# Optimization experiments

Measured on AMD Instinct MI355X. Metric: run time of the kernel, lower is better.

Reference implementation:

```python
import jax, jax.numpy as jnp
import numpy as np

B, L, C, R, DK = 8, 2048, 512, 64, 64
H = 2 * C  # hdnSize
NEG = -32767.0  # -2**15 + 1
EPS = 1e-5


def _p(key, shape, std=0.02):
    return (jax.random.normal(key, shape, dtype=jnp.float32) * std)


def setup_inputs() -> dict:
    key = jax.random.key(0)
    ks = jax.random.split(key, 16)
    inp = {
        "x": jax.random.normal(ks[0], (B, L, C), dtype=jnp.float32),
        "maskPAD": jax.random.randint(ks[1], (B, 1, L), 0, 2, dtype=jnp.int32),
        "preScores": jax.random.normal(ks[2], (B, R, R), dtype=jnp.float32),
        "Wp": _p(ks[3], (C, R)), "bp": jnp.zeros((R,), jnp.float32),
        "Wq": _p(ks[4], (C, DK)), "bq": jnp.zeros((DK,), jnp.float32),
        "Wk": _p(ks[5], (C, DK)), "bk": jnp.zeros((DK,), jnp.float32),
        "Wv": _p(ks[6], (C, H)), "bv": jnp.zeros((H,), jnp.float32),
        "Wu": _p(ks[7], (C, H)), "bu": jnp.zeros((H,), jnp.float32),
        "Wo": _p(ks[8], (H, C)), "bo": jnp.zeros((C,), jnp.float32),
        "gamma": jnp.ones((C,), jnp.float32),
        "beta": jnp.zeros((C,), jnp.float32),
    }
    return inp


def reference(x, maskPAD, preScores, Wp, bp, Wq, bq, Wk, bk, Wv, bv, Wu, bu, Wo, bo, gamma, beta):
    # GLU gate: [B,L,H]
    gate = jax.nn.silu(x @ Wu + bu)
    # pseudo-attention logits [B,L,r], masked on padded positions
    pScore = x @ Wp + bp
    pad = (maskPAD[:, 0] == 0)[..., None]  # [B,L,1]
    pScore = jnp.where(pad, NEG, pScore)
    pAlpha = jax.nn.softmax(pScore, axis=1)    # softmax over L (dim=-2)
    pAlpha_ = jax.nn.softmax(pScore, axis=-1)  # softmax over r
    # compress: px [B,r,C]  (== pAlpha.transpose(-1,-2) @ x)
    px = jnp.einsum('blr,blc->brc', pAlpha, x)
    q = jax.nn.silu(px @ Wq + bq)  # [B,r,dk]
    k = jax.nn.silu(px @ Wk + bk)  # [B,r,dk]
    v = jax.nn.silu(px @ Wv + bv)  # [B,r,H]
    scores = jnp.einsum('brd,bsd->brs', q, k) / np.sqrt(DK).astype(np.float32)
    scores = scores + preScores
    alpha = jax.nn.softmax(scores, axis=2)
    z = alpha @ v                                # [B,r,H]
    z = jnp.einsum('blr,brh->blh', pAlpha_, z)   # expand back to [B,L,H]
    z = gate * z
    z = z @ Wo + bo                              # [B,L,C]
    y = x + z
    mu = jnp.mean(y, axis=-1, keepdims=True)
    var = jnp.var(y, axis=-1, keepdims=True)
    out = (y - mu) * jax.lax.rsqrt(var + EPS) * gamma + beta
    return out
```

## Files before the change

kernel.cpp:

```cpp
#include <hip/hip_runtime.h>
#include <hip/hip_bf16.h>

constexpr int B_ = 8;
constexpr int L_ = 2048;
constexpr int C_ = 512;
constexpr int R_ = 64;
constexpr int DK_ = 64;
constexpr int H_ = 1024;
constexpr int M_ = B_ * L_;
constexpr int NQKV_ = 1152;
constexpr float NEG_ = -32767.0f;

__device__ __forceinline__ float toF(float x) { return x; }
__device__ __forceinline__ float toF(__hip_bfloat16 x) { return __bfloat162float(x); }
__device__ __forceinline__ float siluf(float v) { return v / (1.0f + __expf(-v)); }
__device__ __forceinline__ ushort bfbits(float f) {
    __hip_bfloat16 h = __float2bfloat16(f);
    union { __hip_bfloat16 h; ushort u; } cv; cv.h = h; return cv.u;
}
__device__ __forceinline__ float bf2f(ushort u) {
    union { uint u; float f; } cv; cv.u = (uint)u << 16; return cv.f;
}

typedef __attribute__((ext_vector_type(8))) short bf16x8;
typedef __attribute__((ext_vector_type(4))) float f32x4;

#define GLOBAL_AS __attribute__((address_space(1)))
#define LDS_AS    __attribute__((address_space(3)))
__device__ __forceinline__ void glds16(const ushort* g, ushort* l) {
    __builtin_amdgcn_global_load_lds((const GLOBAL_AS void*)g, (LDS_AS void*)l, 16, 0, 0);
}

#define VMCNT(n) asm volatile("s_waitcnt vmcnt(" #n ")" ::: "memory")
#define BARRIER() do { __builtin_amdgcn_s_barrier(); asm volatile("" ::: "memory"); } while (0)

template <int EPI>
__global__ __launch_bounds__(256) void mfma_gemm5(
    const ushort* __restrict__ A, const ushort* __restrict__ Bt,
    const float* __restrict__ bias,
    const float* __restrict__ residF, const ushort* __restrict__ residB,
    const int* __restrict__ mask,
    ushort* __restrict__ outB, float* __restrict__ outF, float* __restrict__ outF2,
    int Ndim, int Kdim, int gridN, long bBatch)
{
    __shared__ ushort As[3][128 * 32];
    __shared__ ushort Bs[3][128 * 32];

    const int i = blockIdx.x;
    const int G = gridDim.x >> 3;
    const int gi = (gridDim.x & 7) ? i : ((i & 7) * G + (i >> 3));
    const int nt = gi % gridN, mt = gi / gridN;
    const int m0 = mt * 128, n0 = nt * 128;

    const int tid = threadIdx.x;
    const int lane = tid & 63, w = tid >> 6;
    const int wm = (w & 1) * 64, wn = (w >> 1) * 64;
    const int lr = lane & 15, lq = lane >> 4;

    const int sr = lane >> 2;
    const int sc = (lane & 3) * 8;
    const int s0 = w * 2, s1 = w * 2 + 1;

    const ushort* Bp = Bt + (bBatch ? (long)(m0 / L_) * bBatch : 0);
    int br0 = n0 + s0 * 16 + sr; if (br0 >= Ndim) br0 = Ndim - 1;
    int br1 = n0 + s1 * 16 + sr; if (br1 >= Ndim) br1 = Ndim - 1;
    const ushort* a0p = A  + (size_t)(m0 + s0 * 16 + sr) * Kdim + sc;
    const ushort* a1p = A  + (size_t)(m0 + s1 * 16 + sr) * Kdim + sc;
    const ushort* b0p = Bp + (size_t)br0 * Kdim + sc;
    const ushort* b1p = Bp + (size_t)br1 * Kdim + sc;
    const int lo0 = s0 * 512 + lane * 8;
    const int lo1 = s1 * 512 + lane * 8;

    f32x4 acc[4][4];
#pragma unroll
    for (int a = 0; a < 4; ++a)
#pragma unroll
        for (int b = 0; b < 4; ++b) acc[a][b] = (f32x4){0.f, 0.f, 0.f, 0.f};

    glds16(a0p, &As[0][lo0]);
    glds16(a1p, &As[0][lo1]);
    glds16(b0p, &Bs[0][lo0]);
    glds16(b1p, &Bs[0][lo1]);
    if (32 < Kdim) {
        glds16(a0p + 32, &As[1][lo0]);
        glds16(a1p + 32, &As[1][lo1]);
        glds16(b0p + 32, &Bs[1][lo0]);
        glds16(b1p + 32, &Bs[1][lo1]);
    }

    int cur = 0;
    for (int k0 = 0; k0 < Kdim; k0 += 32) {
        if (k0 + 32 < Kdim) VMCNT(4); else VMCNT(0);
        BARRIER();
        if (k0 + 64 < Kdim) {
            const int nx = cur ? cur - 1 : 2;
            glds16(a0p + k0 + 64, &As[nx][lo0]);
            glds16(a1p + k0 + 64, &As[nx][lo1]);
            glds16(b0p + k0 + 64, &Bs[nx][lo0]);
            glds16(b1p + k0 + 64, &Bs[nx][lo1]);
        }
        bf16x8 af[4], bf[4];
#pragma unroll
        for (int a = 0; a < 4; ++a)
            af[a] = *(const bf16x8*)&As[cur][(wm + a * 16 + lr) * 32 + lq * 8];
#pragma unroll
        for (int b = 0; b < 4; ++b)
            bf[b] = *(const bf16x8*)&Bs[cur][(wn + b * 16 + lr) * 32 + lq * 8];
#pragma unroll
        for (int a = 0; a < 4; ++a)
#pragma unroll
            for (int b = 0; b < 4; ++b)
                acc[a][b] = __builtin_amdgcn_mfma_f32_16x16x32_bf16(af[a], bf[b], acc[a][b], 0, 0, 0);
        cur = (cur == 2) ? 0 : cur + 1;
    }

#pragma unroll
    for (int a = 0; a < 4; ++a) {
#pragma unroll
        for (int b = 0; b < 4; ++b) {
            const int col = n0 + wn + b * 16 + lr;
            if (col < Ndim) {
                const float bn = (EPI == 3) ? 0.f : bias[col];
#pragma unroll
                for (int r = 0; r < 4; ++r) {
                    const int row = m0 + wm + a * 16 + lq * 4 + r;
                    float v = acc[a][b][r];
                    if (EPI == 0) {
                        v = siluf(v + bn);
                        outB[(size_t)row * Ndim + col] = bfbits(v);
                    } else if (EPI == 2) {
                        v += bn + residF[(size_t)row * Ndim + col];
                        outB[(size_t)row * Ndim + col] = bfbits(v);
                    } else {
                        v *= bf2f(residB[(size_t)row * Ndim + col]);
                        outB[(size_t)row * Ndim + col] = bfbits(v);
                    }
                }
            }
        }
    }
}

__global__ __launch_bounds__(256) void pscore_gemm(
    const ushort* __restrict__ x16, const ushort* __restrict__ Wpt,
    const float* __restrict__ bp, const int* __restrict__ mask,
    ushort* __restrict__ pAR16, float* __restrict__ pScoreT)
{
    __shared__ ushort As[3][64 * 32];
    __shared__ ushort Bs[3][64 * 32];

    const int i = blockIdx.x;
    const int G = gridDim.x >> 3;
    const int gi = (i & 7) * G + (i >> 3);
    const int m0 = gi * 64;

    const int tid = threadIdx.x;
    const int lane = tid & 63, w = tid >> 6;
    const int lr = lane & 15, lq = lane >> 4;
    const int sr = lane >> 2, sc = (lane & 3) * 8;

    const ushort* ap  = x16 + (size_t)(m0 + w * 16 + sr) * C_ + sc;
    const ushort* bwp = Wpt + (size_t)(w * 16 + sr) * C_ + sc;
    const int loa = w * 512 + lane * 8;

    f32x4 acc[4];
#pragma unroll
    for (int b = 0; b < 4; ++b) acc[b] = (f32x4){0.f, 0.f, 0.f, 0.f};

    glds16(ap, &As[0][loa]);
    glds16(bwp, &Bs[0][loa]);
    glds16(ap + 32, &As[1][loa]);
    glds16(bwp + 32, &Bs[1][loa]);

    int cur = 0;
    for (int k0 = 0; k0 < C_; k0 += 32) {
        if (k0 + 32 < C_) VMCNT(2); else VMCNT(0);
        BARRIER();
        if (k0 + 64 < C_) {
            const int nx = cur ? cur - 1 : 2;
            glds16(ap + k0 + 64, &As[nx][loa]);
            glds16(bwp + k0 + 64, &Bs[nx][loa]);
        }
        bf16x8 af, bf[4];
        af = *(const bf16x8*)&As[cur][(w * 16 + lr) * 32 + lq * 8];
#pragma unroll
        for (int b = 0; b < 4; ++b)
            bf[b] = *(const bf16x8*)&Bs[cur][(b * 16 + lr) * 32 + lq * 8];
#pragma unroll
        for (int b = 0; b < 4; ++b)
            acc[b] = __builtin_amdgcn_mfma_f32_16x16x32_bf16(af, bf[b], acc[b], 0, 0, 0);
        cur = (cur == 2) ? 0 : cur + 1;
    }

#pragma unroll
    for (int r = 0; r < 4; ++r) {
        const int row = m0 + w * 16 + lq * 4 + r;
        const bool dead = (mask[row] == 0);
        const int bb = row >> 11, ll = row & (L_ - 1);
        float v[4];
        float mx = -3.4e38f;
#pragma unroll
        for (int b = 0; b < 4; ++b) {
            const int col = b * 16 + lr;
            float t = acc[b][r] + bp[col];
            if (dead) t = NEG_;
            v[b] = t;
            pScoreT[((size_t)bb * R_ + col) * L_ + ll] = t;
            mx = fmaxf(mx, t);
        }
#pragma unroll
        for (int o = 1; o < 16; o <<= 1) mx = fmaxf(mx, __shfl_xor(mx, o, 64));
        float e[4], s = 0.f;
#pragma unroll
        for (int b = 0; b < 4; ++b) { e[b] = __expf(v[b] - mx); s += e[b]; }
#pragma unroll
        for (int o = 1; o < 16; o <<= 1) s += __shfl_xor(s, o, 64);
        const float inv = 1.0f / s;
#pragma unroll
        for (int b = 0; b < 4; ++b)
            pAR16[(size_t)row * R_ + b * 16 + lr] = bfbits(e[b] * inv);
    }
}

__global__ __launch_bounds__(512) void fused_gate_z(
    const ushort* __restrict__ x16, const ushort* __restrict__ Wut,
    const float* __restrict__ bu,
    const ushort* __restrict__ pAR, const ushort* __restrict__ zsT,
    ushort* __restrict__ zg)
{
    __shared__ ushort As[2][256 * 32];
    __shared__ ushort Bs[2][128 * 32];

    const int i = blockIdx.x;
    const int G = gridDim.x >> 3;
    const int gi = (i & 7) * G + (i >> 3);
    constexpr int gridN = H_ / 128;
    const int nt = gi % gridN, mt = gi / gridN;
    const int m0 = mt * 256, n0 = nt * 128;

    const int tid = threadIdx.x;
    const int lane = tid & 63, w = tid >> 6;
    const int wm = (w & 3) * 64, wn = (w >> 2) * 64;
    const int lr = lane & 15, lq = lane >> 4;
    const int sr = lane >> 2, sc = (lane & 3) * 8;
    const int s0 = w * 2, s1 = w * 2 + 1;

    const int bidx = m0 >> 11;
    const ushort* a0p = x16 + (size_t)(m0 + s0 * 16 + sr) * C_ + sc;
    const ushort* a1p = x16 + (size_t)(m0 + s1 * 16 + sr) * C_ + sc;
    const ushort* b0p = Wut + (size_t)(n0 + w * 16 + sr) * C_ + sc;
    const ushort* zb  = zsT + (size_t)bidx * H_ * R_;
    const ushort* c0p = pAR + (size_t)(m0 + s0 * 16 + sr) * R_ + sc;
    const ushort* c1p = pAR + (size_t)(m0 + s1 * 16 + sr) * R_ + sc;
    const ushort* d0p = zb + (size_t)(n0 + w * 16 + sr) * R_ + sc;
    const int lo0 = s0 * 512 + lane * 8;
    const int lo1 = s1 * 512 + lane * 8;
    const int lob = w * 512 + lane * 8;

    auto stage = [&](int t, int bsel) {
        if (t < 2) {
            const int off = t * 32;
            glds16(c0p + off, &As[bsel][lo0]);
            glds16(c1p + off, &As[bsel][lo1]);
            glds16(d0p + off, &Bs[bsel][lob]);
        } else {
            const int off = (t - 2) * 32;
            glds16(a0p + off, &As[bsel][lo0]);
            glds16(a1p + off, &As[bsel][lo1]);
            glds16(b0p + off, &Bs[bsel][lob]);
        }
    };

    f32x4 acc[4][4];
#pragma unroll
    for (int a = 0; a < 4; ++a)
#pragma unroll
        for (int b = 0; b < 4; ++b) acc[a][b] = (f32x4){0.f, 0.f, 0.f, 0.f};

    uint pk[4][4][2];

    stage(0, 0);

    int cur = 0;
    for (int t = 0; t < 18; ++t) {
        __syncthreads();
        if (t + 1 < 18) stage(t + 1, cur ^ 1);
        bf16x8 af[4], bf[4];
#pragma unroll
        for (int a = 0; a < 4; ++a)
            af[a] = *(const bf16x8*)&As[cur][(wm + a * 16 + lr) * 32 + lq * 8];
#pragma unroll
        for (int b = 0; b < 4; ++b)
            bf[b] = *(const bf16x8*)&Bs[cur][(wn + b * 16 + lr) * 32 + lq * 8];
#pragma unroll
        for (int a = 0; a < 4; ++a)
#pragma unroll
            for (int b = 0; b < 4; ++b)
                acc[a][b] = __builtin_amdgcn_mfma_f32_16x16x32_bf16(af[a], bf[b], acc[a][b], 0, 0, 0);
        if (t == 1) {
#pragma unroll
            for (int a = 0; a < 4; ++a)
#pragma unroll
                for (int b = 0; b < 4; ++b) {
                    pk[a][b][0] = (uint)bfbits(acc[a][b][0]) | ((uint)bfbits(acc[a][b][1]) << 16);
                    pk[a][b][1] = (uint)bfbits(acc[a][b][2]) | ((uint)bfbits(acc[a][b][3]) << 16);
                    acc[a][b] = (f32x4){0.f, 0.f, 0.f, 0.f};
                }
        }
        cur ^= 1;
    }

#pragma unroll
    for (int a = 0; a < 4; ++a) {
#pragma unroll
        for (int b = 0; b < 4; ++b) {
            const int col = n0 + wn + b * 16 + lr;
            const float bn = bu[col];
#pragma unroll
            for (int r = 0; r < 4; ++r) {
                const int row = m0 + wm + a * 16 + lq * 4 + r;
                const ushort zu = (ushort)((r & 1) ? (pk[a][b][r >> 1] >> 16)
                                                   : (pk[a][b][r >> 1] & 0xffff));
                const float v = siluf(acc[a][b][r] + bn) * bf2f(zu);
                zg[(size_t)row * H_ + col] = bfbits(v);
            }
        }
    }
}

__global__ __launch_bounds__(256) void xw_prep(
    const float* __restrict__ x, ushort* __restrict__ x16, ushort* __restrict__ xT16,
    const float* __restrict__ Wu, const float* __restrict__ Wo, const float* __restrict__ Wp,
    const float* __restrict__ Wq, const float* __restrict__ bq,
    const float* __restrict__ Wk, const float* __restrict__ bk,
    const float* __restrict__ Wv, const float* __restrict__ bv,
    ushort* __restrict__ Wut, ushort* __restrict__ Wot, ushort* __restrict__ Wpt,
    ushort* __restrict__ Wqkvt, float* __restrict__ bqkv)
{
    __shared__ float tile[32][33];
    const int tx = threadIdx.x & 31, ty = threadIdx.x >> 5;
    int id = blockIdx.x;

    if (id < 8192) {
        const int c0 = (id & 15) * 32, l0 = (id >> 4) * 32;
#pragma unroll
        for (int i = 0; i < 32; i += 8) {
            const float v = x[(size_t)(l0 + ty + i) * C_ + c0 + tx];
            tile[ty + i][tx] = v;
            x16[(size_t)(l0 + ty + i) * C_ + c0 + tx] = bfbits(v);
        }
        __syncthreads();
        const int bb = l0 >> 11, ll0 = l0 & (L_ - 1);
#pragma unroll
        for (int i = 0; i < 32; i += 8)
            xT16[((size_t)bb * C_ + c0 + ty + i) * L_ + ll0 + tx] = bfbits(tile[tx][ty + i]);
        return;
    }
    id -= 8192;

    const float* W; ushort* Wt; const float* bsrc = nullptr;
    int K, Nloc, n0, k0, nn0;
    if (id < 512) {
        W = Wu; Wt = Wut; K = 512; Nloc = 1024;
        n0 = (id & 31) * 32; k0 = (id >> 5) * 32; nn0 = n0;
    } else if (id < 1024) {
        id -= 512; W = Wo; Wt = Wot; K = 1024; Nloc = 512;
        n0 = (id & 15) * 32; k0 = (id >> 4) * 32; nn0 = n0;
    } else if (id < 1056) {
        id -= 1024; W = Wp; Wt = Wpt; K = 512; Nloc = 64;
        n0 = (id & 1) * 32; k0 = (id >> 1) * 32; nn0 = n0;
    } else {
        id -= 1056; K = 512; Wt = Wqkvt;
        n0 = (id % 36) * 32; k0 = (id / 36) * 32;
        if (n0 < 64)       { W = Wq; bsrc = bq; Nloc = 64;   nn0 = n0; }
        else if (n0 < 128) { W = Wk; bsrc = bk; Nloc = 64;   nn0 = n0 - 64; }
        else               { W = Wv; bsrc = bv; Nloc = 1024; nn0 = n0 - 128; }
    }
#pragma unroll
    for (int i = 0; i < 32; i += 8)
        tile[ty + i][tx] = W[(size_t)(k0 + ty + i) * Nloc + nn0 + tx];
    __syncthreads();
#pragma unroll
    for (int i = 0; i < 32; i += 8)
        Wt[(size_t)(n0 + ty + i) * K + k0 + tx] = bfbits(tile[tx][ty + i]);
    if (bsrc && k0 == 0 && threadIdx.x < 32) bqkv[n0 + threadIdx.x] = bsrc[nn0 + threadIdx.x];
}

__global__ __launch_bounds__(256) void softmaxL2(const float* __restrict__ pScoreT,
                                                 ushort* __restrict__ pALT)
{
    const size_t br = blockIdx.x;
    const float* row = pScoreT + br * L_;
    ushort* orow = pALT + br * L_;
    const int t = threadIdx.x;
    __shared__ float red[256];

    float v[8];
    float mx = -3.4e38f;
#pragma unroll
    for (int j = 0; j < 8; ++j) { v[j] = row[t + j * 256]; mx = fmaxf(mx, v[j]); }
    red[t] = mx; __syncthreads();
    for (int s = 128; s > 0; s >>= 1) { if (t < s) red[t] = fmaxf(red[t], red[t + s]); __syncthreads(); }
    mx = red[0]; __syncthreads();

    float e[8], sum = 0.f;
#pragma unroll
    for (int j = 0; j < 8; ++j) { e[j] = __expf(v[j] - mx); sum += e[j]; }
    red[t] = sum; __syncthreads();
    for (int s = 128; s > 0; s >>= 1) { if (t < s) red[t] += red[t + s]; __syncthreads(); }
    const float inv = 1.0f / red[0];
#pragma unroll
    for (int j = 0; j < 8; ++j) orow[t + j * 256] = bfbits(e[j] * inv);
}

__global__ __launch_bounds__(256) void compress_mfma(
    const ushort* __restrict__ pALT, const ushort* __restrict__ xT,
    float* __restrict__ parts)
{
    __shared__ ushort As[3][64 * 32];
    __shared__ ushort Bs[3][128 * 32];

    const int bidx = blockIdx.y;
    const int n0 = blockIdx.x * 128;
    const int ks = blockIdx.z;
    const int kbeg = ks * (L_ / 8), kend = kbeg + L_ / 8;
    const int tid = threadIdx.x;
    const int lane = tid & 63, w = tid >> 6;
    const int lr = lane & 15, lq = lane >> 4;
    const int sr = lane >> 2, sc = (lane & 3) * 8;
    const int wm = (w & 1) * 32, wn = (w >> 1) * 64;

    const ushort* Ab = pALT + (size_t)bidx * R_ * L_;
    const ushort* Bb = xT + (size_t)bidx * C_ * L_;

    const ushort* ap  = Ab + (size_t)(w * 16 + sr) * L_ + sc;
    const ushort* b0p = Bb + (size_t)(n0 + (2 * w) * 16 + sr) * L_ + sc;
    const ushort* b1p = Bb + (size_t)(n0 + (2 * w + 1) * 16 + sr) * L_ + sc;
    const int alo  = w * 512 + lane * 8;
    const int blo0 = (2 * w) * 512 + lane * 8;
    const int blo1 = (2 * w + 1) * 512 + lane * 8;

    auto stage = [&](int k0, int bsel) {
        glds16(ap + k0, &As[bsel][alo]);
        glds16(b0p + k0, &Bs[bsel][blo0]);
        glds16(b1p + k0, &Bs[bsel][blo1]);
    };

    f32x4 acc[2][4];
#pragma unroll
    for (int a = 0; a < 2; ++a)
#pragma unroll
        for (int b = 0; b < 4; ++b) acc[a][b] = (f32x4){0.f, 0.f, 0.f, 0.f};

    stage(kbeg, 0);
    stage(kbeg + 32, 1);

    int cur = 0;
    for (int k0 = kbeg; k0 < kend; k0 += 32) {
        if (k0 + 32 < kend) VMCNT(3); else VMCNT(0);
        BARRIER();
        if (k0 + 64 < kend) stage(k0 + 64, cur ? cur - 1 : 2);
        bf16x8 af[2], bf[4];
#pragma unroll
        for (int a = 0; a < 2; ++a)
            af[a] = *(const bf16x8*)&As[cur][(wm + a * 16 + lr) * 32 + lq * 8];
#pragma unroll
        for (int b = 0; b < 4; ++b)
            bf[b] = *(const bf16x8*)&Bs[cur][(wn + b * 16 + lr) * 32 + lq * 8];
#pragma unroll
        for (int a = 0; a < 2; ++a)
#pragma unroll
            for (int b = 0; b < 4; ++b)
                acc[a][b] = __builtin_amdgcn_mfma_f32_16x16x32_bf16(af[a], bf[b], acc[a][b], 0, 0, 0);
        cur = (cur == 2) ? 0 : cur + 1;
    }
#pragma unroll
    for (int a = 0; a < 2; ++a)
#pragma unroll
        for (int b = 0; b < 4; ++b)
#pragma unroll
            for (int r = 0; r < 4; ++r) {
                const int row = wm + a * 16 + lq * 4 + r;
                const int col = n0 + wn + b * 16 + lr;
                parts[(((size_t)ks * B_ + bidx) * R_ + row) * C_ + col] = acc[a][b][r];
            }
}

__global__ __launch_bounds__(256) void compress_reduce16(const float* __restrict__ parts,
                                                         ushort* __restrict__ px16)
{
    const size_t i = ((size_t)blockIdx.x * 256 + threadIdx.x) * 4;
    constexpr size_t S = (size_t)B_ * R_ * C_;
    float4 s = *(const float4*)(parts + i);
#pragma unroll
    for (int k = 1; k < 8; ++k) {
        const float4 p = *(const float4*)(parts + i + (size_t)k * S);
        s.x += p.x; s.y += p.y; s.z += p.z; s.w += p.w;
    }
    ushort4 o;
    o.x = bfbits(s.x); o.y = bfbits(s.y); o.z = bfbits(s.z); o.w = bfbits(s.w);
    *(ushort4*)(px16 + i) = o;
}

__global__ __launch_bounds__(256) void attn_fused(
    const ushort* __restrict__ qkv, const float* __restrict__ preS,
    ushort* __restrict__ zsT)
{
    const int b = blockIdx.x >> 6, r = blockIdx.x & 63;
    const int t = threadIdx.x;
    __shared__ float al[R_];
    if (t < 64) {
        const ushort* qr = qkv + (size_t)(b * R_ + r) * NQKV_;
        const ushort* ks = qkv + (size_t)(b * R_ + t) * NQKV_ + 64;
        float acc = 0.f;
#pragma unroll
        for (int d = 0; d < DK_; d += 4) {
            const ushort4 qa = *(const ushort4*)(qr + d);
            const ushort4 ka = *(const ushort4*)(ks + d);
            acc += bf2f(qa.x) * bf2f(ka.x) + bf2f(qa.y) * bf2f(ka.y)
                 + bf2f(qa.z) * bf2f(ka.z) + bf2f(qa.w) * bf2f(ka.w);
        }
        acc = acc * 0.125f + preS[((size_t)b * R_ + r) * R_ + t];
        float mx = acc;
#pragma unroll
        for (int o = 32; o > 0; o >>= 1) mx = fmaxf(mx, __shfl_xor(mx, o, 64));
        float e = __expf(acc - mx);
        float sm = e;
#pragma unroll
        for (int o = 32; o > 0; o >>= 1) sm += __shfl_xor(sm, o, 64);
        al[t] = e / sm;
    }
    __syncthreads();
    float acc[4] = {};
    for (int s = 0; s < R_; ++s) {
        const float a = al[s];
        const ushort* vr = qkv + (size_t)(b * R_ + s) * NQKV_ + 128;
#pragma unroll
        for (int j = 0; j < 4; ++j) acc[j] += a * bf2f(vr[t + j * 256]);
    }
#pragma unroll
    for (int j = 0; j < 4; ++j) {
        const int h = t + j * 256;
        zsT[((size_t)b * H_ + h) * R_ + r] = bfbits(acc[j]);
    }
}

__global__ __launch_bounds__(256) void layernorm(const ushort* __restrict__ y,
                                                 const float* __restrict__ gamma,
                                                 const float* __restrict__ beta,
                                                 float* __restrict__ out)
{
    const int w = threadIdx.x >> 6, lane = threadIdx.x & 63;
    const size_t m = (size_t)blockIdx.x * 4 + w;
    const ushort* yr = y + m * C_ + lane * 8;
    const ushort4 p0 = *(const ushort4*)(yr);
    const ushort4 p1 = *(const ushort4*)(yr + 4);
    float v[8] = { bf2f(p0.x), bf2f(p0.y), bf2f(p0.z), bf2f(p0.w),
                   bf2f(p1.x), bf2f(p1.y), bf2f(p1.z), bf2f(p1.w) };
    float s = 0.f, q = 0.f;
#pragma unroll
    for (int j = 0; j < 8; ++j) { s += v[j]; q += v[j] * v[j]; }
#pragma unroll
    for (int o = 32; o > 0; o >>= 1) {
        s += __shfl_xor(s, o, 64);
        q += __shfl_xor(q, o, 64);
    }
    const float mu = s * (1.0f / C_);
    const float var = q * (1.0f / C_) - mu * mu;
    const float inv = rsqrtf(var + 1e-5f);
    const float4 g0 = *(const float4*)(gamma + lane * 8);
    const float4 g1 = *(const float4*)(gamma + lane * 8 + 4);
    const float4 b0 = *(const float4*)(beta + lane * 8);
    const float4 b1 = *(const float4*)(beta + lane * 8 + 4);
    float4 o0, o1;
    o0.x = (v[0] - mu) * inv * g0.x + b0.x;
    o0.y = (v[1] - mu) * inv * g0.y + b0.y;
    o0.z = (v[2] - mu) * inv * g0.z + b0.z;
    o0.w = (v[3] - mu) * inv * g0.w + b0.w;
    o1.x = (v[4] - mu) * inv * g1.x + b1.x;
    o1.y = (v[5] - mu) * inv * g1.y + b1.y;
    o1.z = (v[6] - mu) * inv * g1.z + b1.z;
    o1.w = (v[7] - mu) * inv * g1.w + b1.w;
    *(float4*)(out + m * C_ + lane * 8) = o0;
    *(float4*)(out + m * C_ + lane * 8 + 4) = o1;
}

template <typename AT, typename BT, typename RT, int ACT, int EPI>
__global__ __launch_bounds__(256) void gemm64(
    const AT* __restrict__ A, const BT* __restrict__ Bw,
    const float* __restrict__ bias, const int* __restrict__ mask,
    const RT* resid, float* __restrict__ outF, __hip_bfloat16* outB,
    int Ndim, int Kdim, long bBatchStride)
{
    __shared__ float As[16][68];
    __shared__ float Bs[16][64];
    const int tid = threadIdx.x;
    const int tx = tid & 15, ty = tid >> 4;
    const int n0 = blockIdx.x * 64, m0 = blockIdx.y * 64;
    const BT* Bp = Bw + (bBatchStride ? (long)(m0 / L_) * bBatchStride : 0);
    float acc[4][4] = {};
    for (int k0 = 0; k0 < Kdim; k0 += 16) {
#pragma unroll
        for (int s = 0; s < 4; ++s) {
            int idx = tid + s * 256;
            int am = idx >> 4, ak = idx & 15;
            As[ak][am] = toF(A[(size_t)(m0 + am) * Kdim + k0 + ak]);
        }
#pragma unroll
        for (int s = 0; s < 4; ++s) {
            int idx = tid + s * 256;
            int bk = idx >> 6, bn = idx & 63;
            Bs[bk][bn] = toF(Bp[(size_t)(k0 + bk) * Ndim + n0 + bn]);
        }
        __syncthreads();
#pragma unroll
        for (int kk = 0; kk < 16; ++kk) {
            float av[4], bv[4];
            *(float4*)av = *(const float4*)&As[kk][ty * 4];
            *(float4*)bv = *(const float4*)&Bs[kk][tx * 4];
#pragma unroll
            for (int i = 0; i < 4; ++i)
#pragma unroll
                for (int j = 0; j < 4; ++j) acc[i][j] += av[i] * bv[j];
        }
        __syncthreads();
    }
#pragma unroll
    for (int i = 0; i < 4; ++i) {
        int m = m0 + ty * 4 + i;
#pragma unroll
        for (int j = 0; j < 4; ++j) {
            int n = n0 + tx * 4 + j;
            float val = acc[i][j];
            if (EPI != 3) val += bias[n];
            if (ACT) val = siluf(val);
            if (EPI == 0) outB[(size_t)m * Ndim + n] = __float2bfloat16(val);
            else if (EPI == 1) { if (mask[m] == 0) val = NEG_; outF[(size_t)m * Ndim + n] = val; }
            else if (EPI == 2) { val += toF(resid[(size_t)m * Ndim + n]); outB[(size_t)m * Ndim + n] = __float2bfloat16(val); }
            else { val *= toF(resid[(size_t)m * Ndim + n]); outB[(size_t)m * Ndim + n] = __float2bfloat16(val); }
        }
    }
}

template <int OUT>
__global__ __launch_bounds__(64) void softmaxR(const float* __restrict__ pScore,
                                               float* __restrict__ outF,
                                               ushort* __restrict__ outU)
{
    const size_t m = blockIdx.x;
    const int t = threadIdx.x;
    float v = pScore[m * R_ + t];
    float mx = v;
#pragma unroll
    for (int o = 32; o > 0; o >>= 1) mx = fmaxf(mx, __shfl_xor(mx, o, 64));
    float e = __expf(v - mx);
    float s = e;
#pragma unroll
    for (int o = 32; o > 0; o >>= 1) s += __shfl_xor(s, o, 64);
    if (OUT == 0) outF[m * R_ + t] = e / s;
    else          outU[m * R_ + t] = bfbits(e / s);
}

__global__ __launch_bounds__(256) void softmaxL(const float* __restrict__ pScore,
                                                float* __restrict__ pAlpha)
{
    const int b = blockIdx.x >> 6, r = blockIdx.x & 63;
    const int t = threadIdx.x;
    const float* base = pScore + (size_t)b * L_ * R_ + r;
    float* out = pAlpha + (size_t)b * L_ * R_ + r;
    __shared__ float red[256];
    float mx = -3.4e38f;
    for (int l = t; l < L_; l += 256) mx = fmaxf(mx, base[(size_t)l * R_]);
    red[t] = mx; __syncthreads();
    for (int s = 128; s > 0; s >>= 1) { if (t < s) red[t] = fmaxf(red[t], red[t + s]); __syncthreads(); }
    mx = red[0]; __syncthreads();
    float sum = 0.f;
    for (int l = t; l < L_; l += 256) {
        float e = __expf(base[(size_t)l * R_] - mx);
        out[(size_t)l * R_] = e; sum += e;
    }
    red[t] = sum; __syncthreads();
    for (int s = 128; s > 0; s >>= 1) { if (t < s) red[t] += red[t + s]; __syncthreads(); }
    const float inv = 1.0f / red[0];
    for (int l = t; l < L_; l += 256) out[(size_t)l * R_] *= inv;
}

__global__ __launch_bounds__(256) void compress_part(
    const float* __restrict__ pAlpha, const float* __restrict__ x,
    float* __restrict__ parts)
{
    __shared__ float As[16][64];
    __shared__ float Bs[16][64];
    const int tid = threadIdx.x;
    const int tx = tid & 15, ty = tid >> 4;
    const int n0 = blockIdx.x * 64;
    const int ks = blockIdx.y;
    const int b  = blockIdx.z;
    const float* pa = pAlpha + (size_t)b * L_ * R_;
    const float* xb = x + (size_t)b * L_ * C_;
    float acc[4][4] = {};
    const int kbeg = ks * (L_ / 4), kend = kbeg + L_ / 4;
    for (int k0 = kbeg; k0 < kend; k0 += 16) {
#pragma unroll
        for (int s = 0; s < 4; ++s) {
            int idx = tid + s * 256;
            int kk = idx >> 6, m = idx & 63;
            As[kk][m] = pa[(size_t)(k0 + kk) * R_ + m];
        }
#pragma unroll
        for (int s = 0; s < 4; ++s) {
            int idx = tid + s * 256;
            int kk = idx >> 6, n = idx & 63;
            Bs[kk][n] = xb[(size_t)(k0 + kk) * C_ + n0 + n];
        }
        __syncthreads();
#pragma unroll
        for (int kk = 0; kk < 16; ++kk) {
            float av[4], bv[4];
            *(float4*)av = *(const float4*)&As[kk][ty * 4];
            *(float4*)bv = *(const float4*)&Bs[kk][tx * 4];
#pragma unroll
            for (int i = 0; i < 4; ++i)
#pragma unroll
                for (int j = 0; j < 4; ++j) acc[i][j] += av[i] * bv[j];
        }
        __syncthreads();
    }
#pragma unroll
    for (int i = 0; i < 4; ++i)
#pragma unroll
        for (int j = 0; j < 4; ++j)
            parts[((((size_t)ks * B_ + b) * R_) + ty * 4 + i) * C_ + n0 + tx * 4 + j] = acc[i][j];
}

__global__ __launch_bounds__(256) void compress_reduce(const float* __restrict__ parts,
                                                       float* __restrict__ px)
{
    const size_t i = (size_t)blockIdx.x * 256 + threadIdx.x;
    constexpr size_t S = (size_t)B_ * R_ * C_;
    px[i] = parts[i] + parts[i + S] + parts[i + 2 * S] + parts[i + 3 * S];
}

__global__ __launch_bounds__(256) void qkv_gemm(
    const float* __restrict__ px,
    const float* __restrict__ Wq, const float* __restrict__ bq,
    const float* __restrict__ Wk, const float* __restrict__ bk,
    const float* __restrict__ Wv, const float* __restrict__ bv,
    float* __restrict__ q, float* __restrict__ k, float* __restrict__ v)
{
    __shared__ float As[16][68];
    __shared__ float Bs[16][64];
    const int tid = threadIdx.x;
    const int tx = tid & 15, ty = tid >> 4;
    const int bx = blockIdx.x;
    const int m0 = blockIdx.y * 64;
    const float* W; const float* bias; float* dst; int Nloc, ncol0;
    if (bx == 0)      { W = Wq; bias = bq; dst = q; Nloc = 64;   ncol0 = 0; }
    else if (bx == 1) { W = Wk; bias = bk; dst = k; Nloc = 64;   ncol0 = 0; }
    else              { W = Wv; bias = bv; dst = v; Nloc = H_;   ncol0 = (bx - 2) * 64; }

    float acc[4][4] = {};
    for (int k0 = 0; k0 < C_; k0 += 16) {
#pragma unroll
        for (int s = 0; s < 4; ++s) {
            int idx = tid + s * 256;
            int am = idx >> 4, ak = idx & 15;
            As[ak][am] = px[(size_t)(m0 + am) * C_ + k0 + ak];
        }
#pragma unroll
        for (int s = 0; s < 4; ++s) {
            int idx = tid + s * 256;
            int kk = idx >> 6, bn = idx & 63;
            Bs[kk][bn] = W[(size_t)(k0 + kk) * Nloc + ncol0 + bn];
        }
        __syncthreads();
#pragma unroll
        for (int kk = 0; kk < 16; ++kk) {
            float av[4], bv4[4];
            *(float4*)av = *(const float4*)&As[kk][ty * 4];
            *(float4*)bv4 = *(const float4*)&Bs[kk][tx * 4];
#pragma unroll
            for (int i = 0; i < 4; ++i)
#pragma unroll
                for (int j = 0; j < 4; ++j) acc[i][j] += av[i] * bv4[j];
        }
        __syncthreads();
    }
#pragma unroll
    for (int i = 0; i < 4; ++i) {
        int m = m0 + ty * 4 + i;
#pragma unroll
        for (int j = 0; j < 4; ++j) {
            int n = ncol0 + tx * 4 + j;
            dst[(size_t)m * Nloc + n] = siluf(acc[i][j] + bias[n]);
        }
    }
}

template <int MODE>
__global__ __launch_bounds__(256) void attn_z(const float* __restrict__ alpha,
                                              const float* __restrict__ v,
                                              float* __restrict__ zsF,
                                              ushort* __restrict__ zsT)
{
    const int b = blockIdx.x >> 6, r = blockIdx.x & 63;
    const int t = threadIdx.x;
    __shared__ float al[R_];
    if (t < R_) al[t] = alpha[((size_t)b * R_ + r) * R_ + t];
    __syncthreads();
    float acc[4] = {};
    for (int s = 0; s < R_; ++s) {
        float a = al[s];
        const float* vr = v + ((size_t)b * R_ + s) * H_;
#pragma unroll
        for (int j = 0; j < 4; ++j) acc[j] += a * vr[t + j * 256];
    }
#pragma unroll
    for (int j = 0; j < 4; ++j) {
        const int h = t + j * 256;
        if (MODE == 0) zsF[((size_t)b * R_ + r) * H_ + h] = acc[j];
        else           zsT[((size_t)b * H_ + h) * R_ + r] = bfbits(acc[j]);
    }
}

__global__ __launch_bounds__(64) void attn_scores(
    const float* __restrict__ q, const float* __restrict__ k,
    const float* __restrict__ preS, float* __restrict__ alpha)
{
    const int b = blockIdx.x >> 6, r = blockIdx.x & 63;
    const int s = threadIdx.x;
    const float* qr = q + ((size_t)b * R_ + r) * DK_;
    const float* ks = k + ((size_t)b * R_ + s) * DK_;
    float acc = 0.f;
#pragma unroll
    for (int d = 0; d < DK_; ++d) acc += qr[d] * ks[d];
    acc = acc * 0.125f + preS[((size_t)b * R_ + r) * R_ + s];
    float mx = acc;
#pragma unroll
    for (int o = 32; o > 0; o >>= 1) mx = fmaxf(mx, __shfl_xor(mx, o, 64));
    float e = __expf(acc - mx);
    float sm = e;
#pragma unroll
    for (int o = 32; o > 0; o >>= 1) sm += __shfl_xor(sm, o, 64);
    alpha[((size_t)b * R_ + r) * R_ + s] = e / sm;
}

extern "C" void kernel_launch(void* const* d_in, const int* in_sizes, int n_in,
                              void* d_out, int out_size, void* d_ws, size_t ws_size,
                              hipStream_t stream)
{
    using bf16 = __hip_bfloat16;
    const float* x      = (const float*)d_in[0];
    const int*  maskPAD = (const int*)d_in[1];
    const float* preS   = (const float*)d_in[2];
    const float* Wp     = (const float*)d_in[3];
    const float* bp     = (const float*)d_in[4];
    const float* Wq     = (const float*)d_in[5];
    const float* bq     = (const float*)d_in[6];
    const float* Wk     = (const float*)d_in[7];
    const float* bk     = (const float*)d_in[8];
    const float* Wv     = (const float*)d_in[9];
    const float* bv     = (const float*)d_in[10];
    const float* Wu     = (const float*)d_in[11];
    const float* bu     = (const float*)d_in[12];
    const float* Wo     = (const float*)d_in[13];
    const float* bo     = (const float*)d_in[14];
    const float* gamma  = (const float*)d_in[15];
    const float* beta   = (const float*)d_in[16];
    float* out          = (float*)d_out;

    char* ws = (char*)d_ws;
    const bool bigWS = ws_size >= (size_t)52 * 1024 * 1024;

    if (bigWS) {
        bf16* zg = (bf16*)ws;
        float* parts = (float*)ws;
        char* pool = ws + (size_t)M_ * H_ * 2;
        float* pScoreT = (float*)pool;
        ushort* pALT   = (ushort*)(pScoreT + (size_t)B_ * R_ * L_);
        ushort* pAR16  = pALT + (size_t)B_ * R_ * L_;
        ushort* px16   = pAR16 + (size_t)M_ * R_;
        ushort* qkv16  = px16 + (size_t)B_ * R_ * C_;
        ushort* zsT16  = qkv16 + (size_t)B_ * R_ * NQKV_;
        ushort* Wqkvt  = zsT16 + (size_t)B_ * H_ * R_;
        float*  bqkv   = (float*)(Wqkvt + (size_t)NQKV_ * C_);
        bf16*  y       = (bf16*)pool;
        ushort* Wut    = (ushort*)(pool + 18221568);
        ushort* Wot    = Wut + (size_t)C_ * H_;
        ushort* Wpt    = Wot + (size_t)C_ * H_;
        ushort* x16    = (ushort*)d_out;
        ushort* xT16   = x16 + (size_t)M_ * C_;

        xw_prep<<<8192 + 1632, 256, 0, stream>>>(
            x, x16, xT16, Wu, Wo, Wp, Wq, bq, Wk, bk, Wv, bv,
            Wut, Wot, Wpt, Wqkvt, bqkv);
        pscore_gemm<<<M_ / 64, 256, 0, stream>>>(x16, Wpt, bp, maskPAD, pAR16, pScoreT);
        softmaxL2<<<B_ * R_, 256, 0, stream>>>(pScoreT, pALT);
        compress_mfma<<<dim3(C_ / 128, B_, 8), 256, 0, stream>>>(pALT, xT16, parts);
        compress_reduce16<<<(B_ * R_ * C_) / 1024, 256, 0, stream>>>(parts, px16);
        mfma_gemm5<0><<<(NQKV_ / 128) * ((B_ * R_) / 128), 256, 0, stream>>>(
            px16, Wqkvt, bqkv, nullptr, nullptr, nullptr, qkv16, nullptr, nullptr,
            NQKV_, C_, NQKV_ / 128, 0);
        attn_fused<<<B_ * R_, 256, 0, stream>>>(qkv16, preS, zsT16);
        fused_gate_z<<<(H_ / 128) * (M_ / 256), 512, 0, stream>>>(
            x16, Wut, bu, pAR16, zsT16, (ushort*)zg);
        mfma_gemm5<2><<<(C_ / 128) * (M_ / 128), 256, 0, stream>>>(
            (ushort*)zg, Wot, bo, x, nullptr, nullptr, (ushort*)y, nullptr, nullptr,
            C_, H_, C_ / 128, 0);
        layernorm<<<M_ / 4, 256, 0, stream>>>((const ushort*)y, gamma, beta, out);
    } else {
        float* pScore = (float*)ws;
        float* pAL   = pScore + (size_t)M_ * R_;
        float* pAR   = pAL    + (size_t)M_ * R_;
        float* px    = pAR    + (size_t)M_ * R_;
        float* q     = px     + (size_t)B_ * R_ * C_;
        float* kk    = q      + (size_t)B_ * R_ * DK_;
        float* vv    = kk     + (size_t)B_ * R_ * DK_;
        float* alpha = vv     + (size_t)B_ * R_ * H_;
        float* zs    = alpha  + (size_t)B_ * R_ * R_;
        bf16* gate_b = (bf16*)(zs + (size_t)B_ * R_ * H_);
        bf16* y_b    = (bf16*)((char*)gate_b + (size_t)L_ * H_ * 2);

        gemm64<float, float, float, 0, 1><<<dim3(R_ / 64, M_ / 64), 256, 0, stream>>>(
            x, Wp, bp, maskPAD, (const float*)nullptr, pScore, nullptr, R_, C_, 0);
        softmaxL<<<B_ * R_, 256, 0, stream>>>(pScore, pAL);
        softmaxR<0><<<M_, 64, 0, stream>>>(pScore, pAR, nullptr);
        compress_part<<<dim3(C_ / 64, 4, B_), 256, 0, stream>>>(pAL, x, pScore);
        compress_reduce<<<(B_ * R_ * C_) / 256, 256, 0, stream>>>(pScore, px);
        qkv_gemm<<<dim3(2 + H_ / 64, (B_ * R_) / 64), 256, 0, stream>>>(
            px, Wq, bq, Wk, bk, Wv, bv, q, kk, vv);
        attn_scores<<<B_ * R_, 64, 0, stream>>>(q, kk, preS, alpha);
        attn_z<0><<<B_ * R_, 256, 0, stream>>>(alpha, vv, zs, nullptr);

        for (int b = 0; b < B_; ++b) {
            const float* xb = x + (size_t)b * L_ * C_;
            gemm64<float, float, float, 1, 0><<<dim3(H_ / 64, L_ / 64), 256, 0, stream>>>(
                xb, Wu, bu, nullptr, (const float*)nullptr, nullptr, gate_b, H_, C_, 0);
            gemm64<float, float, bf16, 0, 3><<<dim3(H_ / 64, L_ / 64), 256, 0, stream>>>(
                pAR + (size_t)b * L_ * R_, zs + (size_t)b * R_ * H_,
                nullptr, nullptr, gate_b, nullptr, gate_b, H_, R_, 0);
            gemm64<bf16, float, float, 0, 2><<<dim3(C_ / 64, L_ / 64), 256, 0, stream>>>(
                gate_b, Wo, bo, nullptr, xb, nullptr, y_b, C_, H_, 0);
            layernorm<<<L_ / 4, 256, 0, stream>>>((const ushort*)y_b, gamma, beta, out + (size_t)b * L_ * C_);
        }
    }
}
```

Baseline: 256.4 us.

## Fuse softmax over L into pscore GEMM with deferred normalization; retile QKV GEMM

The pscore GEMM now writes unnormalized exp(score) as bf16 to pALT and atomically accumulates per-(batch, r) column sums. The normalization is deferred to compress_reduce16, which divides by those sums, so the separate softmaxL2 kernel and its fp32 pScoreT round trip are removed. The QKV projection moves to a dedicated 64x64-tile kernel, giving more blocks for the small M=512 problem. The risk is that skipping the max subtraction assumes scores are small enough not to overflow exp, and the atomics add nondeterminism to the sums.

New measurement: 246.7 us. 3.8% less time.

```diff
diff --git a/kernel.cpp b/kernel.cpp
--- a/kernel.cpp
+++ b/kernel.cpp
@@ -144,7 +144,8 @@
 __global__ __launch_bounds__(256) void pscore_gemm(
     const ushort* __restrict__ x16, const ushort* __restrict__ Wpt,
     const float* __restrict__ bp, const int* __restrict__ mask,
-    ushort* __restrict__ pAR16, float* __restrict__ pScoreT)
+    ushort* __restrict__ pAR16, ushort* __restrict__ pALT,
+    float* __restrict__ sums)
 {
     __shared__ ushort As[3][64 * 32];
     __shared__ ushort Bs[3][64 * 32];
@@ -192,11 +193,13 @@
         cur = (cur == 2) ? 0 : cur + 1;
     }
 
+    const int bb = m0 >> 11;
+    float colsum[4] = {0.f, 0.f, 0.f, 0.f};
 #pragma unroll
     for (int r = 0; r < 4; ++r) {
         const int row = m0 + w * 16 + lq * 4 + r;
         const bool dead = (mask[row] == 0);
-        const int bb = row >> 11, ll = row & (L_ - 1);
+        const int ll = row & (L_ - 1);
         float v[4];
         float mx = -3.4e38f;
 #pragma unroll
@@ -205,8 +208,10 @@
             float t = acc[b][r] + bp[col];
             if (dead) t = NEG_;
             v[b] = t;
-            pScoreT[((size_t)bb * R_ + col) * L_ + ll] = t;
             mx = fmaxf(mx, t);
+            const float eL = __expf(t);
+            colsum[b] += eL;
+            pALT[((size_t)bb * R_ + col) * L_ + ll] = bfbits(eL);
         }
 #pragma unroll
         for (int o = 1; o < 16; o <<= 1) mx = fmaxf(mx, __shfl_xor(mx, o, 64));
@@ -219,6 +224,75 @@
 #pragma unroll
         for (int b = 0; b < 4; ++b)
             pAR16[(size_t)row * R_ + b * 16 + lr] = bfbits(e[b] * inv);
+    }
+#pragma unroll
+    for (int b = 0; b < 4; ++b) {
+        colsum[b] += __shfl_xor(colsum[b], 16, 64);
+        colsum[b] += __shfl_xor(colsum[b], 32, 64);
+    }
+    if (lq == 0) {
+#pragma unroll
+        for (int b = 0; b < 4; ++b)
+            atomicAdd(&sums[bb * R_ + b * 16 + lr], colsum[b]);
+    }
+}
+
+__global__ __launch_bounds__(256) void qkv64(
+    const ushort* __restrict__ px16, const ushort* __restrict__ Wqkvt,
+    const float* __restrict__ bqkv, ushort* __restrict__ qkv16)
+{
+    __shared__ ushort As[3][64 * 32];
+    __shared__ ushort Bs[3][64 * 32];
+
+    const int nt = blockIdx.x % 18, mt = blockIdx.x / 18;
+    const int m0 = mt * 64, n0 = nt * 64;
+
+    const int tid = threadIdx.x;
+    const int lane = tid & 63, w = tid >> 6;
+    const int lr = lane & 15, lq = lane >> 4;
+    const int sr = lane >> 2, sc = (lane & 3) * 8;
+
+    const ushort* ap  = px16 + (size_t)(m0 + w * 16 + sr) * C_ + sc;
+    const ushort* bwp = Wqkvt + (size_t)(n0 + w * 16 + sr) * C_ + sc;
+    const int loa = w * 512 + lane * 8;
+
+    f32x4 acc[4];
+#pragma unroll
+    for (int b = 0; b < 4; ++b) acc[b] = (f32x4){0.f, 0.f, 0.f, 0.f};
+
+    glds16(ap, &As[0][loa]);
+    glds16(bwp, &Bs[0][loa]);
+    glds16(ap + 32, &As[1][loa]);
+    glds16(bwp + 32, &Bs[1][loa]);
+
+    int cur = 0;
+    for (int k0 = 0; k0 < C_; k0 += 32) {
+        if (k0 + 32 < C_) VMCNT(2); else VMCNT(0);
+        BARRIER();
+        if (k0 + 64 < C_) {
+            const int nx = cur ? cur - 1 : 2;
+            glds16(ap + k0 + 64, &As[nx][loa]);
+            glds16(bwp + k0 + 64, &Bs[nx][loa]);
+        }
+        bf16x8 af, bf[4];
+        af = *(const bf16x8*)&As[cur][(w * 16 + lr) * 32 + lq * 8];
+#pragma unroll
+        for (int b = 0; b < 4; ++b)
+            bf[b] = *(const bf16x8*)&Bs[cur][(b * 16 + lr) * 32 + lq * 8];
+#pragma unroll
+        for (int b = 0; b < 4; ++b)
+            acc[b] = __builtin_amdgcn_mfma_f32_16x16x32_bf16(af, bf[b], acc[b], 0, 0, 0);
+        cur = (cur == 2) ? 0 : cur + 1;
+    }
+
+#pragma unroll
+    for (int r = 0; r < 4; ++r) {
+        const int row = m0 + w * 16 + lq * 4 + r;
+#pragma unroll
+        for (int b = 0; b < 4; ++b) {
+            const int col = n0 + b * 16 + lr;
+            qkv16[(size_t)row * NQKV_ + col] = bfbits(siluf(acc[b][r] + bqkv[col]));
+        }
     }
 }
 
@@ -335,11 +409,17 @@
     const float* __restrict__ Wk, const float* __restrict__ bk,
     const float* __restrict__ Wv, const float* __restrict__ bv,
     ushort* __restrict__ Wut, ushort* __restrict__ Wot, ushort* __restrict__ Wpt,
-    ushort* __restrict__ Wqkvt, float* __restrict__ bqkv)
+    ushort* __restrict__ Wqkvt, float* __restrict__ bqkv, float* __restrict__ sums)
 {
     __shared__ float tile[32][33];
     const int tx = threadIdx.x & 31, ty = threadIdx.x >> 5;
     int id = blockIdx.x;
+
+    if (id == 8192 + 1632) {
+        sums[threadIdx.x] = 0.f;
+        sums[threadIdx.x + 256] = 0.f;
+        return;
+    }
 
     if (id < 8192) {
         const int c0 = (id & 15) * 32, l0 = (id >> 4) * 32;
@@ -386,33 +466,6 @@
     if (bsrc && k0 == 0 && threadIdx.x < 32) bqkv[n0 + threadIdx.x] = bsrc[nn0 + threadIdx.x];
 }
 
-__global__ __launch_bounds__(256) void softmaxL2(const float* __restrict__ pScoreT,
-                                                 ushort* __restrict__ pALT)
-{
-    const size_t br = blockIdx.x;
-    const float* row = pScoreT + br * L_;
-    ushort* orow = pALT + br * L_;
-    const int t = threadIdx.x;
-    __shared__ float red[256];
-
-    float v[8];
-    float mx = -3.4e38f;
-#pragma unroll
-    for (int j = 0; j < 8; ++j) { v[j] = row[t + j * 256]; mx = fmaxf(mx, v[j]); }
-    red[t] = mx; __syncthreads();
-    for (int s = 128; s > 0; s >>= 1) { if (t < s) red[t] = fmaxf(red[t], red[t + s]); __syncthreads(); }
-    mx = red[0]; __syncthreads();
-
-    float e[8], sum = 0.f;
-#pragma unroll
-    for (int j = 0; j < 8; ++j) { e[j] = __expf(v[j] - mx); sum += e[j]; }
-    red[t] = sum; __syncthreads();
-    for (int s = 128; s > 0; s >>= 1) { if (t < s) red[t] += red[t + s]; __syncthreads(); }
-    const float inv = 1.0f / red[0];
-#pragma unroll
-    for (int j = 0; j < 8; ++j) orow[t + j * 256] = bfbits(e[j] * inv);
-}
-
 __global__ __launch_bounds__(256) void compress_mfma(
     const ushort* __restrict__ pALT, const ushort* __restrict__ xT,
     float* __restrict__ parts)
@@ -487,6 +540,7 @@
 }
 
 __global__ __launch_bounds__(256) void compress_reduce16(const float* __restrict__ parts,
+                                                         const float* __restrict__ sums,
                                                          ushort* __restrict__ px16)
 {
     const size_t i = ((size_t)blockIdx.x * 256 + threadIdx.x) * 4;
@@ -497,8 +551,10 @@
         const float4 p = *(const float4*)(parts + i + (size_t)k * S);
         s.x += p.x; s.y += p.y; s.z += p.z; s.w += p.w;
     }
+    const float inv = 1.0f / sums[i / C_];
     ushort4 o;
-    o.x = bfbits(s.x); o.y = bfbits(s.y); o.z = bfbits(s.z); o.w = bfbits(s.w);
+    o.x = bfbits(s.x * inv); o.y = bfbits(s.y * inv);
+    o.z = bfbits(s.z * inv); o.w = bfbits(s.w * inv);
     *(ushort4*)(px16 + i) = o;
 }
 
@@ -876,14 +932,14 @@
         bf16* zg = (bf16*)ws;
         float* parts = (float*)ws;
         char* pool = ws + (size_t)M_ * H_ * 2;
-        float* pScoreT = (float*)pool;
-        ushort* pALT   = (ushort*)(pScoreT + (size_t)B_ * R_ * L_);
+        ushort* pALT   = (ushort*)pool;
         ushort* pAR16  = pALT + (size_t)B_ * R_ * L_;
         ushort* px16   = pAR16 + (size_t)M_ * R_;
         ushort* qkv16  = px16 + (size_t)B_ * R_ * C_;
         ushort* zsT16  = qkv16 + (size_t)B_ * R_ * NQKV_;
         ushort* Wqkvt  = zsT16 + (size_t)B_ * H_ * R_;
         float*  bqkv   = (float*)(Wqkvt + (size_t)NQKV_ * C_);
+        float*  sums   = bqkv + NQKV_;
         bf16*  y       = (bf16*)pool;
         ushort* Wut    = (ushort*)(pool + 18221568);
         ushort* Wot    = Wut + (size_t)C_ * H_;
@@ -891,16 +947,14 @@
         ushort* x16    = (ushort*)d_out;
         ushort* xT16   = x16 + (size_t)M_ * C_;
 
-        xw_prep<<<8192 + 1632, 256, 0, stream>>>(
+        xw_prep<<<8192 + 1632 + 1, 256, 0, stream>>>(
             x, x16, xT16, Wu, Wo, Wp, Wq, bq, Wk, bk, Wv, bv,
-            Wut, Wot, Wpt, Wqkvt, bqkv);
-        pscore_gemm<<<M_ / 64, 256, 0, stream>>>(x16, Wpt, bp, maskPAD, pAR16, pScoreT);
-        softmaxL2<<<B_ * R_, 256, 0, stream>>>(pScoreT, pALT);
+            Wut, Wot, Wpt, Wqkvt, bqkv, sums);
+        pscore_gemm<<<M_ / 64, 256, 0, stream>>>(x16, Wpt, bp, maskPAD,
+                                                 pAR16, pALT, sums);
         compress_mfma<<<dim3(C_ / 128, B_, 8), 256, 0, stream>>>(pALT, xT16, parts);
-        compress_reduce16<<<(B_ * R_ * C_) / 1024, 256, 0, stream>>>(parts, px16);
-        mfma_gemm5<0><<<(NQKV_ / 128) * ((B_ * R_) / 128), 256, 0, stream>>>(
-            px16, Wqkvt, bqkv, nullptr, nullptr, nullptr, qkv16, nullptr, nullptr,
-            NQKV_, C_, NQKV_ / 128, 0);
+        compress_reduce16<<<(B_ * R_ * C_) / 1024, 256, 0, stream>>>(parts, sums, px16);
+        qkv64<<<(B_ * R_ / 64) * (NQKV_ / 64), 256, 0, stream>>>(px16, Wqkvt, bqkv, qkv16);
         attn_fused<<<B_ * R_, 256, 0, stream>>>(qkv16, preS, zsT16);
         fused_gate_z<<<(H_ / 128) * (M_ / 256), 512, 0, stream>>>(
             x16, Wut, bu, pAR16, zsT16, (ushort*)zg);
```
